# Optimization experiments

Measured on AMD Instinct MI355X. Metric: run time of the kernel, lower is better.

The kernel has to match this reference:

```python
import jax, jax.numpy as jnp
import numpy as np

INF = 100000000.0
NUM_CLASSES = 80
RADIUS = 1.5

_SHAPES = [(100, 152), (50, 76), (25, 38), (13, 19), (7, 10)]
_STRIDES = [8, 16, 32, 64, 128]
_SOI = [(-1.0, 64.0), (64.0, 128.0), (128.0, 256.0), (256.0, 512.0), (512.0, INF)]


def _build_locations():
    locs, strs, sizes = [], [], []
    for (h, w), s, (lo, hi) in zip(_SHAPES, _STRIDES, _SOI):
        sx = np.arange(0, w * s, s, dtype=np.float32)
        sy = np.arange(0, h * s, s, dtype=np.float32)
        yy, xx = np.meshgrid(sy, sx, indexing='ij')
        l = np.stack([xx.ravel(), yy.ravel()], axis=1) + s // 2
        locs.append(l)
        strs.append(np.full(h * w, s, dtype=np.float32))
        sizes.append(np.tile(np.array([lo, hi], np.float32), (h * w, 1)))
    return (np.concatenate(locs, 0), np.concatenate(strs, 0), np.concatenate(sizes, 0))


def setup_inputs() -> dict:
    key = jax.random.key(0)
    locs, str_per, soi = _build_locations()  # K=20267
    B, G = 8, 64
    k1, k2, k3, k4 = jax.random.split(key, 4)
    cx = jax.random.uniform(k1, (B, G), minval=50.0, maxval=1150.0)
    cy = jax.random.uniform(k2, (B, G), minval=50.0, maxval=750.0)
    wh = jax.random.uniform(k3, (B, G, 2), minval=16.0, maxval=400.0)
    gt_boxes = jnp.stack([cx - wh[..., 0] / 2, cy - wh[..., 1] / 2,
                          cx + wh[..., 0] / 2, cy + wh[..., 1] / 2], axis=-1)
    gt_classes = jax.random.randint(k4, (B, G), 0, NUM_CLASSES)
    locations = jnp.asarray(locs)
    strides_per_loc = jnp.asarray(str_per)
    sizes_of_interest = jnp.asarray(soi)
    # FCOS-style single anchor per location: box centered at location, side = 4*stride
    anchors = jnp.concatenate([locations - 2.0 * strides_per_loc[:, None],
                               locations + 2.0 * strides_per_loc[:, None]], axis=-1)
    return {"locations": locations, "strides_per_loc": strides_per_loc,
            "sizes_of_interest": sizes_of_interest, "anchors": anchors,
            "gt_boxes": gt_boxes, "gt_classes": gt_classes}


def reference(locations, strides_per_loc, sizes_of_interest, anchors, gt_boxes, gt_classes):
    xs, ys = locations[:, 0], locations[:, 1]  # [K]

    def per_image(boxes, classes):
        # boxes [G,4], classes [G]
        l = xs[:, None] - boxes[None, :, 0]
        t = ys[:, None] - boxes[None, :, 1]
        r = boxes[None, :, 2] - xs[:, None]
        b = boxes[None, :, 3] - ys[:, None]
        reg = jnp.stack([l, t, r, b], axis=2)  # [K,G,4]
        # center sampling (get_sample_region), vectorized over per-location stride
        ccx = (boxes[:, 0] + boxes[:, 2]) / 2
        ccy = (boxes[:, 1] + boxes[:, 3]) / 2
        rad = (strides_per_loc * RADIUS)[:, None]  # [K,1]
        xmin = jnp.maximum(ccx[None, :] - rad, boxes[None, :, 0])
        ymin = jnp.maximum(ccy[None, :] - rad, boxes[None, :, 1])
        xmax = jnp.minimum(ccx[None, :] + rad, boxes[None, :, 2])
        ymax = jnp.minimum(ccy[None, :] + rad, boxes[None, :, 3])
        cb_min = jnp.minimum(jnp.minimum(xs[:, None] - xmin, ys[:, None] - ymin),
                             jnp.minimum(xmax - xs[:, None], ymax - ys[:, None]))
        in_box = cb_min > 0  # [K,G]
        max_reg = reg.max(axis=2)  # [K,G]
        cared = (max_reg >= sizes_of_interest[:, 0:1]) & (max_reg <= sizes_of_interest[:, 1:2])
        area = (boxes[:, 2] - boxes[:, 0]) * (boxes[:, 3] - boxes[:, 1])  # [G]
        loc2area = jnp.where(in_box & cared, area[None, :], INF)  # masked-fill with INF
        min_area = loc2area.min(axis=1)
        inds = jnp.argmin(loc2area, axis=1)  # [K], first min like torch
        cls = jnp.where(min_area == INF, NUM_CLASSES, classes[inds])
        reg_t = jnp.take_along_axis(reg, inds[:, None, None], axis=1)[:, 0, :]  # [K,4]
        matched = boxes[inds]  # [K,4]
        # Box2BoxTransform.get_deltas with unit weights
        aw = anchors[:, 2] - anchors[:, 0]
        ah = anchors[:, 3] - anchors[:, 1]
        acx = anchors[:, 0] + 0.5 * aw
        acy = anchors[:, 1] + 0.5 * ah
        gw = matched[:, 2] - matched[:, 0]
        gh = matched[:, 3] - matched[:, 1]
        gcx = matched[:, 0] + 0.5 * gw
        gcy = matched[:, 1] + 0.5 * gh
        deltas = jnp.stack([(gcx - acx) / aw, (gcy - acy) / ah,
                            jnp.log(gw / aw), jnp.log(gh / ah)], axis=1)  # [K,4]
        return cls, reg_t, deltas

    gt_cls, reg_targets, gt_deltas = jax.vmap(per_image)(gt_boxes, gt_classes)
    return gt_cls, reg_targets, gt_deltas
```

## Files before the change

### kernel.cpp

```cpp
#include <hip/hip_runtime.h>

#define NGT 64
#define NUM_CLASSES_F 80.0f
#define INF_F 100000000.0f
#define RADIUS_F 1.5f

__global__ __launch_bounds__(256) void fcos_match_kernel(
    const float* __restrict__ locations,
    const float* __restrict__ strides_per_loc,
    const float* __restrict__ soi,
    const float* __restrict__ anchors,
    const float* __restrict__ gt_boxes,
    const int*   __restrict__ gt_classes,
    float* __restrict__ out,
    int L, int B)
{
    const int b = blockIdx.y;
    const int i = blockIdx.x * blockDim.x + threadIdx.x;

    __shared__ float4 sbox[NGT];
    __shared__ float  sarea[NGT];
    __shared__ float  sccx[NGT];
    __shared__ float  sccy[NGT];
    __shared__ float  sclsf[NGT];

    if (threadIdx.x < NGT) {
        const int j = threadIdx.x;
        float4 bx = reinterpret_cast<const float4*>(gt_boxes)[b * NGT + j];
        sbox[j]  = bx;
        sarea[j] = (bx.z - bx.x) * (bx.w - bx.y);
        sccx[j]  = (bx.x + bx.z) * 0.5f;
        sccy[j]  = (bx.y + bx.w) * 0.5f;
        sclsf[j] = (float)gt_classes[b * NGT + j];
    }
    __syncthreads();

    if (i >= L) return;

    const float2 xy = reinterpret_cast<const float2*>(locations)[i];
    const float  x  = xy.x, y = xy.y;
    const float  rad = strides_per_loc[i] * RADIUS_F;
    const float2 lohi = reinterpret_cast<const float2*>(soi)[i];
    const float  lo = lohi.x, hi = lohi.y;

    float minv = INF_F;
    int   ind  = 0;

    #pragma unroll
    for (int j = 0; j < NGT; ++j) {
        const float4 bx = sbox[j];
        const float l  = x - bx.x;
        const float t  = y - bx.y;
        const float r  = bx.z - x;
        const float bb = bx.w - y;

        const float xmin = fmaxf(sccx[j] - rad, bx.x);
        const float ymin = fmaxf(sccy[j] - rad, bx.y);
        const float xmax = fminf(sccx[j] + rad, bx.z);
        const float ymax = fminf(sccy[j] + rad, bx.w);

        const float cb = fminf(fminf(x - xmin, y - ymin),
                               fminf(xmax - x, ymax - y));
        const float mx = fmaxf(fmaxf(l, t), fmaxf(r, bb));

        const bool valid = (cb > 0.0f) && (mx >= lo) && (mx <= hi);
        const float v = valid ? sarea[j] : INF_F;
        if (v < minv) { minv = v; ind = j; }
    }

    const float4 mb = sbox[ind];
    const float l  = x - mb.x;
    const float t  = y - mb.y;
    const float r  = mb.z - x;
    const float bb = mb.w - y;

    const float cls = (minv == INF_F) ? NUM_CLASSES_F : sclsf[ind];
    out[(size_t)b * L + i] = cls;

    const size_t reg_base = (size_t)B * L + ((size_t)b * L + i) * 4;
    out[reg_base + 0] = l;
    out[reg_base + 1] = t;
    out[reg_base + 2] = r;
    out[reg_base + 3] = bb;

    const float4 an = reinterpret_cast<const float4*>(anchors)[i];
    const float aw  = an.z - an.x;
    const float ah  = an.w - an.y;
    const float acx = an.x + 0.5f * aw;
    const float acy = an.y + 0.5f * ah;
    const float gw  = mb.z - mb.x;
    const float gh  = mb.w - mb.y;
    const float gcx = mb.x + 0.5f * gw;
    const float gcy = mb.y + 0.5f * gh;

    const size_t del_base = (size_t)B * L * 5 + ((size_t)b * L + i) * 4;
    out[del_base + 0] = (gcx - acx) / aw;
    out[del_base + 1] = (gcy - acy) / ah;
    out[del_base + 2] = logf(gw / aw);
    out[del_base + 3] = logf(gh / ah);
}

extern "C" void kernel_launch(void* const* d_in, const int* in_sizes, int n_in,
                              void* d_out, int out_size, void* d_ws, size_t ws_size,
                              hipStream_t stream) {
    const float* locations = (const float*)d_in[0];
    const float* strides   = (const float*)d_in[1];
    const float* soi       = (const float*)d_in[2];
    const float* anchors   = (const float*)d_in[3];
    const float* gt_boxes  = (const float*)d_in[4];
    const int*   gt_cls    = (const int*)d_in[5];
    float* out = (float*)d_out;

    const int L = in_sizes[1];
    const int B = in_sizes[5] / NGT;

    dim3 block(256);
    dim3 grid((L + 255) / 256, B);
    fcos_match_kernel<<<grid, block, 0, stream>>>(locations, strides, soi, anchors,
                                                  gt_boxes, gt_cls, out, L, B);
}
```

Measured before the change: 16.43 us.

## Precompute GT box table in setup kernel and read it via uniform loads

Adds a small setup kernel that packs each GT box with its center, area and class into an 8-float table in workspace. The match kernel drops its shared-memory staging and __syncthreads and reads the table directly with block-uniform indices, which the compiler can turn into scalar loads. Output stores for regression targets and deltas become float4 vector stores. The cost is an extra kernel launch, and the loop now depends on scalar cache loads instead of LDS.

```diff
diff --git a/kernel.cpp b/kernel.cpp
--- a/kernel.cpp
+++ b/kernel.cpp
@@ -5,83 +5,82 @@
 #define INF_F 100000000.0f
 #define RADIUS_F 1.5f
 
+__global__ void fcos_setup_kernel(const float* __restrict__ gt_boxes,
+                                  const int* __restrict__ gt_classes,
+                                  float* __restrict__ tb, int BG)
+{
+    const int t = blockIdx.x * blockDim.x + threadIdx.x;
+    if (t >= BG) return;
+    const float4 bx = reinterpret_cast<const float4*>(gt_boxes)[t];
+    float4* e = reinterpret_cast<float4*>(tb + (size_t)t * 8);
+    e[0] = bx;
+    e[1] = make_float4((bx.x + bx.z) * 0.5f,
+                       (bx.y + bx.w) * 0.5f,
+                       (bx.z - bx.x) * (bx.w - bx.y),
+                       (float)gt_classes[t]);
+}
+
 __global__ __launch_bounds__(256) void fcos_match_kernel(
     const float* __restrict__ locations,
     const float* __restrict__ strides_per_loc,
     const float* __restrict__ soi,
     const float* __restrict__ anchors,
-    const float* __restrict__ gt_boxes,
-    const int*   __restrict__ gt_classes,
+    const float* __restrict__ tb,
     float* __restrict__ out,
     int L, int B)
 {
     const int b = blockIdx.y;
     const int i = blockIdx.x * blockDim.x + threadIdx.x;
-
-    __shared__ float4 sbox[NGT];
-    __shared__ float  sarea[NGT];
-    __shared__ float  sccx[NGT];
-    __shared__ float  sccy[NGT];
-    __shared__ float  sclsf[NGT];
-
-    if (threadIdx.x < NGT) {
-        const int j = threadIdx.x;
-        float4 bx = reinterpret_cast<const float4*>(gt_boxes)[b * NGT + j];
-        sbox[j]  = bx;
-        sarea[j] = (bx.z - bx.x) * (bx.w - bx.y);
-        sccx[j]  = (bx.x + bx.z) * 0.5f;
-        sccy[j]  = (bx.y + bx.w) * 0.5f;
-        sclsf[j] = (float)gt_classes[b * NGT + j];
-    }
-    __syncthreads();
-
     if (i >= L) return;
 
-    const float2 xy = reinterpret_cast<const float2*>(locations)[i];
-    const float  x  = xy.x, y = xy.y;
-    const float  rad = strides_per_loc[i] * RADIUS_F;
+    const float2 xy   = reinterpret_cast<const float2*>(locations)[i];
+    const float  x    = xy.x, y = xy.y;
+    const float  rad  = strides_per_loc[i] * RADIUS_F;
     const float2 lohi = reinterpret_cast<const float2*>(soi)[i];
-    const float  lo = lohi.x, hi = lohi.y;
+
+    const float* __restrict__ bt = tb + (size_t)b * NGT * 8;
 
     float minv = INF_F;
     int   ind  = 0;
 
     #pragma unroll
     for (int j = 0; j < NGT; ++j) {
-        const float4 bx = sbox[j];
-        const float l  = x - bx.x;
-        const float t  = y - bx.y;
-        const float r  = bx.z - x;
-        const float bb = bx.w - y;
+        const float bx0  = bt[j * 8 + 0];
+        const float by0  = bt[j * 8 + 1];
+        const float bx1  = bt[j * 8 + 2];
+        const float by1  = bt[j * 8 + 3];
+        const float ccx  = bt[j * 8 + 4];
+        const float ccy  = bt[j * 8 + 5];
+        const float area = bt[j * 8 + 6];
 
-        const float xmin = fmaxf(sccx[j] - rad, bx.x);
-        const float ymin = fmaxf(sccy[j] - rad, bx.y);
-        const float xmax = fminf(sccx[j] + rad, bx.z);
-        const float ymax = fminf(sccy[j] + rad, bx.w);
-
-        const float cb = fminf(fminf(x - xmin, y - ymin),
-                               fminf(xmax - x, ymax - y));
+        const float l  = x - bx0;
+        const float t  = y - by0;
+        const float r  = bx1 - x;
+        const float bb = by1 - y;
         const float mx = fmaxf(fmaxf(l, t), fmaxf(r, bb));
 
-        const bool valid = (cb > 0.0f) && (mx >= lo) && (mx <= hi);
-        const float v = valid ? sarea[j] : INF_F;
+        const float xmin = fmaxf(ccx - rad, bx0);
+        const float ymin = fmaxf(ccy - rad, by0);
+        const float xmax = fminf(ccx + rad, bx1);
+        const float ymax = fminf(ccy + rad, by1);
+        const float cb   = fminf(fminf(x - xmin, y - ymin),
+                                 fminf(xmax - x, ymax - y));
+
+        const float g = fminf(mx - lohi.x, lohi.y - mx);
+        const bool valid = (cb > 0.0f) && (g >= 0.0f);
+        const float v = valid ? area : INF_F;
         if (v < minv) { minv = v; ind = j; }
     }
 
-    const float4 mb = sbox[ind];
-    const float l  = x - mb.x;
-    const float t  = y - mb.y;
-    const float r  = mb.z - x;
-    const float bb = mb.w - y;
+    const float4* me = reinterpret_cast<const float4*>(bt + ind * 8);
+    const float4 mb = me[0];
+    const float4 md = me[1];
 
-    const float cls = (minv == INF_F) ? NUM_CLASSES_F : sclsf[ind];
-    out[(size_t)b * L + i] = cls;
+    out[(size_t)b * L + i] = (minv == INF_F) ? NUM_CLASSES_F : md.w;
 
-    const size_t reg_base = (size_t)B * L + ((size_t)b * L + i) * 4;
-    out[reg_base + 0] = l;
-    out[reg_base + 1] = t;
-    out[reg_base + 2] = r;
-    out[reg_base + 3] = bb;
+    const size_t o4 = (size_t)b * L + i;
+    float4* reg4 = reinterpret_cast<float4*>(out + (size_t)B * L) + o4;
+    *reg4 = make_float4(x - mb.x, y - mb.y, mb.z - x, mb.w - y);
 
     const float4 an = reinterpret_cast<const float4*>(anchors)[i];
     const float aw  = an.z - an.x;
@@ -93,11 +92,9 @@
     const float gcx = mb.x + 0.5f * gw;
     const float gcy = mb.y + 0.5f * gh;
 
-    const size_t del_base = (size_t)B * L * 5 + ((size_t)b * L + i) * 4;
-    out[del_base + 0] = (gcx - acx) / aw;
-    out[del_base + 1] = (gcy - acy) / ah;
-    out[del_base + 2] = logf(gw / aw);
-    out[del_base + 3] = logf(gh / ah);
+    float4* del4 = reinterpret_cast<float4*>(out + (size_t)B * L * 5) + o4;
+    *del4 = make_float4((gcx - acx) / aw, (gcy - acy) / ah,
+                        logf(gw / aw), logf(gh / ah));
 }
 
 extern "C" void kernel_launch(void* const* d_in, const int* in_sizes, int n_in,
@@ -110,12 +107,15 @@
     const float* gt_boxes  = (const float*)d_in[4];
     const int*   gt_cls    = (const int*)d_in[5];
     float* out = (float*)d_out;
+    float* tb  = (float*)d_ws;
 
-    const int L = in_sizes[1];
-    const int B = in_sizes[5] / NGT;
+    const int L  = in_sizes[1];
+    const int BG = in_sizes[5];
+    const int B  = BG / NGT;
 
-    dim3 block(256);
+    fcos_setup_kernel<<<(BG + 255) / 256, 256, 0, stream>>>(gt_boxes, gt_cls, tb, BG);
+
     dim3 grid((L + 255) / 256, B);
-    fcos_match_kernel<<<grid, block, 0, stream>>>(locations, strides, soi, anchors,
-                                                  gt_boxes, gt_cls, out, L, B);
+    fcos_match_kernel<<<grid, dim3(256), 0, stream>>>(locations, strides, soi, anchors,
+                                                      tb, out, L, B);
 }
```

New measurement: 25.42 us. +54.7%, slower.

## Split GT loop across thread pairs with shuffle argmin and vector stores

Applied to the files above, without the earlier changes.

Each location is now handled by two adjacent threads, each scanning 32 of the 64 GT boxes, and the two partial minima are merged with a lane-xor shuffle that keeps the first index on ties. The output work is also split: one thread writes the class and regression target, the other computes the deltas, with float4 stores in place of scalar stores. The per-box center-sampling test is rewritten with abs-based distances, and area and centers are recomputed in the loop rather than read from shared memory. This doubles the thread count and shortens the serial loop, in exchange for more blocks, a shuffle, and divergent epilogue branches.

```diff
diff --git a/kernel.cpp b/kernel.cpp
--- a/kernel.cpp
+++ b/kernel.cpp
@@ -16,88 +16,81 @@
     int L, int B)
 {
     const int b = blockIdx.y;
-    const int i = blockIdx.x * blockDim.x + threadIdx.x;
 
     __shared__ float4 sbox[NGT];
-    __shared__ float  sarea[NGT];
-    __shared__ float  sccx[NGT];
-    __shared__ float  sccy[NGT];
     __shared__ float  sclsf[NGT];
-
     if (threadIdx.x < NGT) {
         const int j = threadIdx.x;
-        float4 bx = reinterpret_cast<const float4*>(gt_boxes)[b * NGT + j];
-        sbox[j]  = bx;
-        sarea[j] = (bx.z - bx.x) * (bx.w - bx.y);
-        sccx[j]  = (bx.x + bx.z) * 0.5f;
-        sccy[j]  = (bx.y + bx.w) * 0.5f;
+        sbox[j]  = reinterpret_cast<const float4*>(gt_boxes)[b * NGT + j];
         sclsf[j] = (float)gt_classes[b * NGT + j];
     }
     __syncthreads();
 
-    if (i >= L) return;
+    const int  k      = threadIdx.x & 1;
+    const int  p      = blockIdx.x * 128 + (threadIdx.x >> 1);
+    const bool active = p < L;
+    const int  i      = active ? p : 0;
 
-    const float2 xy = reinterpret_cast<const float2*>(locations)[i];
-    const float  x  = xy.x, y = xy.y;
-    const float  rad = strides_per_loc[i] * RADIUS_F;
+    const float2 xy   = reinterpret_cast<const float2*>(locations)[i];
+    const float  x    = xy.x, y = xy.y;
+    const float  rad  = strides_per_loc[i] * RADIUS_F;
     const float2 lohi = reinterpret_cast<const float2*>(soi)[i];
-    const float  lo = lohi.x, hi = lohi.y;
 
     float minv = INF_F;
-    int   ind  = 0;
+    int   ind  = k << 5;
 
     #pragma unroll
-    for (int j = 0; j < NGT; ++j) {
-        const float4 bx = sbox[j];
-        const float l  = x - bx.x;
-        const float t  = y - bx.y;
-        const float r  = bx.z - x;
-        const float bb = bx.w - y;
+    for (int j = 0; j < 32; ++j) {
+        const int jg = (k << 5) | j;
+        const float4 bx = sbox[jg];
 
-        const float xmin = fmaxf(sccx[j] - rad, bx.x);
-        const float ymin = fmaxf(sccy[j] - rad, bx.y);
-        const float xmax = fminf(sccx[j] + rad, bx.z);
-        const float ymax = fminf(sccy[j] + rad, bx.w);
+        const float l = x - bx.x, t = y - bx.y;
+        const float r = bx.z - x, d = bx.w - y;
+        const float mx = fmaxf(fmaxf(fmaxf(l, t), r), d);
+        const float mn = fminf(fminf(fminf(l, t), r), d);
 
-        const float cb = fminf(fminf(x - xmin, y - ymin),
-                               fminf(xmax - x, ymax - y));
-        const float mx = fmaxf(fmaxf(l, t), fmaxf(r, bb));
+        const float ccx = (bx.x + bx.z) * 0.5f;
+        const float ccy = (bx.y + bx.w) * 0.5f;
+        const float cx  = rad - fabsf(x - ccx);
+        const float cy  = rad - fabsf(y - ccy);
+        const float cmin = fminf(fminf(mn, cx), cy);
 
-        const bool valid = (cb > 0.0f) && (mx >= lo) && (mx <= hi);
-        const float v = valid ? sarea[j] : INF_F;
-        if (v < minv) { minv = v; ind = j; }
+        const float g    = fminf(mx - lohi.x, lohi.y - mx);
+        const float area = (bx.z - bx.x) * (bx.w - bx.y);
+        const float v = ((cmin > 0.0f) && (g >= 0.0f)) ? area : INF_F;
+        if (v < minv) { minv = v; ind = jg; }
     }
 
+    const float vp   = __shfl_xor(minv, 1);
+    const int   indp = __shfl_xor(ind, 1);
+    const bool  take = (vp < minv) || ((vp == minv) && (k != 0));
+    minv = take ? vp : minv;
+    ind  = take ? indp : ind;
+
+    if (!active) return;
+
     const float4 mb = sbox[ind];
-    const float l  = x - mb.x;
-    const float t  = y - mb.y;
-    const float r  = mb.z - x;
-    const float bb = mb.w - y;
+    const size_t o4 = (size_t)b * L + i;
 
-    const float cls = (minv == INF_F) ? NUM_CLASSES_F : sclsf[ind];
-    out[(size_t)b * L + i] = cls;
+    if (k == 0) {
+        out[o4] = (minv == INF_F) ? NUM_CLASSES_F : sclsf[ind];
+        float4* reg4 = reinterpret_cast<float4*>(out + (size_t)B * L) + o4;
+        *reg4 = make_float4(x - mb.x, y - mb.y, mb.z - x, mb.w - y);
+    } else {
+        const float4 an = reinterpret_cast<const float4*>(anchors)[i];
+        const float aw  = an.z - an.x;
+        const float ah  = an.w - an.y;
+        const float acx = an.x + 0.5f * aw;
+        const float acy = an.y + 0.5f * ah;
+        const float gw  = mb.z - mb.x;
+        const float gh  = mb.w - mb.y;
+        const float gcx = mb.x + 0.5f * gw;
+        const float gcy = mb.y + 0.5f * gh;
 
-    const size_t reg_base = (size_t)B * L + ((size_t)b * L + i) * 4;
-    out[reg_base + 0] = l;
-    out[reg_base + 1] = t;
-    out[reg_base + 2] = r;
-    out[reg_base + 3] = bb;
-
-    const float4 an = reinterpret_cast<const float4*>(anchors)[i];
-    const float aw  = an.z - an.x;
-    const float ah  = an.w - an.y;
-    const float acx = an.x + 0.5f * aw;
-    const float acy = an.y + 0.5f * ah;
-    const float gw  = mb.z - mb.x;
-    const float gh  = mb.w - mb.y;
-    const float gcx = mb.x + 0.5f * gw;
-    const float gcy = mb.y + 0.5f * gh;
-
-    const size_t del_base = (size_t)B * L * 5 + ((size_t)b * L + i) * 4;
-    out[del_base + 0] = (gcx - acx) / aw;
-    out[del_base + 1] = (gcy - acy) / ah;
-    out[del_base + 2] = logf(gw / aw);
-    out[del_base + 3] = logf(gh / ah);
+        float4* del4 = reinterpret_cast<float4*>(out + (size_t)B * L * 5) + o4;
+        *del4 = make_float4((gcx - acx) / aw, (gcy - acy) / ah,
+                            logf(gw / aw), logf(gh / ah));
+    }
 }
 
 extern "C" void kernel_launch(void* const* d_in, const int* in_sizes, int n_in,
@@ -114,8 +107,7 @@
     const int L = in_sizes[1];
     const int B = in_sizes[5] / NGT;
 
-    dim3 block(256);
-    dim3 grid((L + 255) / 256, B);
-    fcos_match_kernel<<<grid, block, 0, stream>>>(locations, strides, soi, anchors,
-                                                  gt_boxes, gt_cls, out, L, B);
+    dim3 grid((L + 127) / 128, B);
+    fcos_match_kernel<<<grid, dim3(256), 0, stream>>>(locations, strides, soi, anchors,
+                                                      gt_boxes, gt_cls, out, L, B);
 }
```

Measured after the change: 14.35 us. -12.6%, faster.
